# Performance work log

Measured on AMD Instinct MI355X. Metric: run time of the kernel, lower is better.

The kernel has to match this reference:

```python
import jax, jax.numpy as jnp
import numpy as np

TOPK = 8
N_EXPERTS = 64
ALPHA = 0.001


def setup_inputs() -> dict:
    key = jax.random.key(0)
    k1, k2 = jax.random.split(key)
    B, S, H = 4, 4096, 4096
    x = jax.random.normal(k1, (B, S, H), dtype=jnp.float32)
    # kaiming-uniform-ish router weight, bound = sqrt(6/((1+5)*H)) = 1/sqrt(H)
    bound = 1.0 / np.sqrt(H)
    weight = jax.random.uniform(k2, (N_EXPERTS, H), dtype=jnp.float32,
                                minval=-bound, maxval=bound)
    return {"x": x, "weight": weight}


def reference(x, weight):
    B, S, H = x.shape
    E = weight.shape[0]
    tokens = x.reshape(-1, H)                      # (T, H), T = B*S
    logits = jnp.einsum('th,eh->te', tokens, weight)  # router GEMM (T, E)
    scores = jax.nn.softmax(logits, axis=-1)
    # top-k selection (torch uses sorted=False; same set of values/indices)
    topk_weight, topk_idx = jax.lax.top_k(scores, TOPK)  # (T, k)
    # normalize top-k probs (norm_topk_prob=True, topk>1)
    topk_weight = topk_weight / (topk_weight.sum(axis=1, keepdims=True) + 1e-20)
    # seq-aux load-balancing loss (training path, alpha > 0, seq_aux=True)
    idx_flat = topk_idx.reshape(B, S * TOPK)                 # (B, S*k)
    ce = jax.nn.one_hot(idx_flat, E, dtype=jnp.float32).sum(axis=1)  # scatter_add of ones
    ce = ce / (S * TOPK / E)                                  # (B, E)
    mean_scores = scores.reshape(B, S, E).mean(axis=1)        # (B, E)
    aux_loss = (ce * mean_scores).sum(axis=1).mean() * ALPHA
    return topk_idx, topk_weight, aux_loss
```

## Files before the change

### kernel.cpp

```cpp
#include <hip/hip_runtime.h>
#include <math.h>

#define H 4096
#define NE 64
#define KTOP 8
#define BT 64
#define TTOT 16384
#define NBLK (TTOT / BT)
#define TAU 1e-4f
#define DELTA 1e-3f

typedef __attribute__((ext_vector_type(8))) short bf16x8;
typedef __attribute__((ext_vector_type(4))) float f32x4;

union U4S8 { uint4 u; bf16x8 s; };

__device__ __forceinline__ unsigned bf16_rne(float f) {
  unsigned b = __float_as_uint(f);
  b += 0x7fffu + ((b >> 16) & 1u);
  return b >> 16;
}

__global__ __launch_bounds__(256) void w_prep(const float* __restrict__ w,
                                              uint4* __restrict__ wsimg) {
  const int sid = blockIdx.x * 256 + threadIdx.x;
  const int e = sid >> 9;
  const int rem = sid & 511;
  const int c = rem >> 2;
  const int s = rem & 3;
  const float* src = w + (size_t)e * H + c * 32 + s * 8;
  float4 f0 = *(const float4*)src;
  float4 f1 = *(const float4*)(src + 4);
  float xf[8] = {f0.x, f0.y, f0.z, f0.w, f1.x, f1.y, f1.z, f1.w};
  unsigned hu[8], lu[8];
#pragma unroll
  for (int j = 0; j < 8; ++j) {
    hu[j] = bf16_rne(xf[j]);
    float hf = __uint_as_float(hu[j] << 16);
    lu[j] = bf16_rne(xf[j] - hf);
  }
  uint4 hp, lp;
  hp.x = hu[0] | (hu[1] << 16); hp.y = hu[2] | (hu[3] << 16);
  hp.z = hu[4] | (hu[5] << 16); hp.w = hu[6] | (hu[7] << 16);
  lp.x = lu[0] | (lu[1] << 16); lp.y = lu[2] | (lu[3] << 16);
  lp.z = lu[4] | (lu[5] << 16); lp.w = lu[6] | (lu[7] << 16);
  const int slotp = s ^ ((e >> 1) & 3);
  wsimg[(size_t)c * 256 + e * 4 + slotp] = hp;
  wsimg[(size_t)128 * 256 + (size_t)c * 256 + e * 4 + slotp] = lp;
}

struct __align__(16) SmemP1 {
  uint4 wbuf[2][1024];
  float lg[64 * 66];
  float msum[8][64];
  float cnt[8][64];
};

__global__ __launch_bounds__(512) void moe_pass1(
    const float* __restrict__ x, const uint4* __restrict__ wsimg,
    float* __restrict__ out, unsigned* __restrict__ wmask,
    float* __restrict__ waux) {
  __shared__ SmemP1 sm;
  const int tid = threadIdx.x;
  const int lane = tid & 63;
  const int wid = tid >> 6;
  const int tile = wid & 3;
  const int kh = wid >> 2;
  const int tok0 = blockIdx.x * BT;
  const int trow = lane & 15;
  const int kgrp = lane >> 4;

  const int sh = tid >> 8;
  const int shl = (tid >> 7) & 1;
  const int sfl = tid & 127;
  const uint4* simg = wsimg + (size_t)shl * (128 * 256);
  const int sdst = (sh * 2 + shl) * 256 + sfl * 2;

  const float* xp = x + (size_t)(tok0 + tile * 16 + trow) * H + kh * 2048 + kgrp * 8;

  int bidx[2][4];
#pragma unroll
  for (int hl = 0; hl < 2; ++hl)
#pragma unroll
    for (int et = 0; et < 4; ++et) {
      int e = et * 16 + trow;
      bidx[hl][et] = (kh * 2 + hl) * 256 + e * 4 + (kgrp ^ ((e >> 1) & 3));
    }

  f32x4 acc[4];
#pragma unroll
  for (int et = 0; et < 4; ++et) acc[et] = (f32x4){0.f, 0.f, 0.f, 0.f};

  {
    const int cg = sh ? 64 : 0;
    uint4 a = simg[(size_t)cg * 256 + sfl * 2];
    uint4 b = simg[(size_t)cg * 256 + sfl * 2 + 1];
    sm.wbuf[0][sdst] = a;
    sm.wbuf[0][sdst + 1] = b;
  }
  float4 xc0 = *(const float4*)(xp);
  float4 xc1 = *(const float4*)(xp + 4);
  __syncthreads();

#pragma unroll 1
  for (int c = 0; c < 64; ++c) {
    uint4 wg0, wg1;
    float4 xn0, xn1;
    const bool more = (c + 1) < 64;
    if (more) {
      const int cg = (sh ? 64 : 0) + c + 1;
      wg0 = simg[(size_t)cg * 256 + sfl * 2];
      wg1 = simg[(size_t)cg * 256 + sfl * 2 + 1];
      xn0 = *(const float4*)(xp + (c + 1) * 32);
      xn1 = *(const float4*)(xp + (c + 1) * 32 + 4);
    }
    const int buf = c & 1;
    U4S8 bh[4], bl[4];
#pragma unroll
    for (int et = 0; et < 4; ++et) {
      bh[et].u = sm.wbuf[buf][bidx[0][et]];
      bl[et].u = sm.wbuf[buf][bidx[1][et]];
    }
    float xf[8] = {xc0.x, xc0.y, xc0.z, xc0.w, xc1.x, xc1.y, xc1.z, xc1.w};
    unsigned ph[4], pl[4];
#pragma unroll
    for (int q = 0; q < 4; ++q)
      asm("v_cvt_pk_bf16_f32 %0, %1, %2" : "=v"(ph[q]) : "v"(xf[2 * q]), "v"(xf[2 * q + 1]));
    float rs[8];
#pragma unroll
    for (int q = 0; q < 4; ++q) {
      rs[2 * q]     = xf[2 * q]     - __uint_as_float(ph[q] << 16);
      rs[2 * q + 1] = xf[2 * q + 1] - __uint_as_float(ph[q] & 0xffff0000u);
    }
#pragma unroll
    for (int q = 0; q < 4; ++q)
      asm("v_cvt_pk_bf16_f32 %0, %1, %2" : "=v"(pl[q]) : "v"(rs[2 * q]), "v"(rs[2 * q + 1]));
    U4S8 ah, al;
    ah.u = (uint4){ph[0], ph[1], ph[2], ph[3]};
    al.u = (uint4){pl[0], pl[1], pl[2], pl[3]};
#pragma unroll
    for (int et = 0; et < 4; ++et) {
      acc[et] = __builtin_amdgcn_mfma_f32_16x16x32_bf16(ah.s, bh[et].s, acc[et], 0, 0, 0);
      acc[et] = __builtin_amdgcn_mfma_f32_16x16x32_bf16(ah.s, bl[et].s, acc[et], 0, 0, 0);
      acc[et] = __builtin_amdgcn_mfma_f32_16x16x32_bf16(al.s, bh[et].s, acc[et], 0, 0, 0);
    }
    if (more) {
      sm.wbuf[buf ^ 1][sdst] = wg0;
      sm.wbuf[buf ^ 1][sdst + 1] = wg1;
      xc0 = xn0; xc1 = xn1;
    }
    __syncthreads();
  }

  if (kh == 1) {
#pragma unroll
    for (int et = 0; et < 4; ++et)
#pragma unroll
      for (int r = 0; r < 4; ++r)
        sm.lg[(tile * 16 + kgrp * 4 + r) * 66 + et * 16 + trow] = acc[et][r];
  }
  __syncthreads();
  if (kh == 0) {
#pragma unroll
    for (int et = 0; et < 4; ++et)
#pragma unroll
      for (int r = 0; r < 4; ++r) {
        const int li = (tile * 16 + kgrp * 4 + r) * 66 + et * 16 + trow;
        sm.lg[li] += acc[et][r];
      }
  }
  __syncthreads();

  float msum = 0.f;
  int cnt = 0;
#pragma unroll 1
  for (int it = 0; it < 8; ++it) {
    const int t = wid * 8 + it;
    const float lf = sm.lg[t * 66 + lane];

    float m = lf;
#pragma unroll
    for (int off = 32; off; off >>= 1) m = fmaxf(m, __shfl_xor(m, off));
    float p = expf(lf - m);
    float s = p;
#pragma unroll
    for (int off = 32; off; off >>= 1) s += __shfl_xor(s, off);
    msum += p / s;

    float cur = lf;
    float myv = 0.f;
    int myi = 0;
#pragma unroll
    for (int r = 0; r < 9; ++r) {
      float v = cur;
      int ix = lane;
#pragma unroll
      for (int off = 1; off < 64; off <<= 1) {
        float ov = __shfl_xor(v, off);
        int oi = __shfl_xor(ix, off);
        if (ov > v || (ov == v && oi < ix)) { v = ov; ix = oi; }
      }
      if (lane == r) { myv = v; myi = ix; }
      if (r < 8 && lane == ix) { cur = -INFINITY; ++cnt; }
    }

    const float m0 = __shfl(myv, 0);
    float e = expf(myv - m0);
    float sv = e;
    sv += __shfl_xor(sv, 1);
    sv += __shfl_xor(sv, 2);
    sv += __shfl_xor(sv, 4);
    const float wgtv = e / sv;
    const int tg = tok0 + t;
    if (lane < KTOP) {
      out[(size_t)tg * KTOP + lane] = (float)myi;
      out[(size_t)TTOT * KTOP + (size_t)tg * KTOP + lane] = wgtv;
    }

    const float nxt = __shfl(myv, (lane + 1) & 63);
    const bool gp = (lane < 8) && (myv - nxt < TAU);
    const unsigned long long anyg = __ballot(gp);
    const float v7 = __shfl(myv, 7);
    const unsigned long long msk = __ballot(lf >= v7 - DELTA);
    if (lane == 0) {
      const unsigned long long mv = anyg ? msk : 0ULL;
      wmask[tg] = (unsigned)mv;
      wmask[TTOT + tg] = (unsigned)(mv >> 32);
    }
  }
  sm.msum[wid][lane] = msum;
  sm.cnt[wid][lane] = (float)cnt;
  __syncthreads();
  if (tid < 64) {
    float c8 = 0.f, m8 = 0.f;
#pragma unroll
    for (int k = 0; k < 8; ++k) { c8 += sm.cnt[k][tid]; m8 += sm.msum[k][tid]; }
    waux[blockIdx.x * 128 + tid] = c8;
    waux[blockIdx.x * 128 + 64 + tid] = m8;
  }
}

__global__ __launch_bounds__(256) void moe_pass2(
    const float* __restrict__ x, const float* __restrict__ w,
    const unsigned* __restrict__ wmask, float* __restrict__ out) {
  __shared__ unsigned slo[64], shi[64];
  __shared__ double red[4];
  __shared__ double cval[64];
  __shared__ int cidx[64];
  const int tid = threadIdx.x;
  const int lane = tid & 63, wid = tid >> 6;
  const int t0 = blockIdx.x * BT;

  if (tid < 64) { slo[tid] = wmask[t0 + tid]; shi[tid] = wmask[TTOT + t0 + tid]; }
  __syncthreads();
  int myf = (tid < 64) ? ((slo[tid] | shi[tid]) != 0u) : 0;
  if (!__syncthreads_or(myf)) return;

#pragma unroll 1
  for (int tt = 0; tt < BT; ++tt) {
    const unsigned lo = slo[tt], hi = shi[tt];
    if (!(lo | hi)) continue;
    const int t = t0 + tt;
    const unsigned long long m = ((unsigned long long)hi << 32) | lo;
    const float* xr = x + (size_t)t * H;
    int ncand = 0;
#pragma unroll 1
    for (int e = 0; e < 64; ++e) {
      if (!((m >> e) & 1ULL)) continue;
      const float* wr = w + (size_t)e * H;
      double d = 0.0;
#pragma unroll
      for (int q = 0; q < 16; ++q) {
        const int k = tid + 256 * q;
        d = fma((double)xr[k], (double)wr[k], d);
      }
#pragma unroll
      for (int off = 32; off; off >>= 1) d += __shfl_xor(d, off);
      if (lane == 0) red[wid] = d;
      __syncthreads();
      if (tid == 0) {
        cval[ncand] = red[0] + red[1] + red[2] + red[3];
        cidx[ncand] = e;
      }
      __syncthreads();
      ++ncand;
    }
    if (tid == 0) {
      double sel[8];
      int si[8];
      for (int r = 0; r < 8; ++r) {
        int best = 0;
        double bv = -1e300;
        for (int c2 = 0; c2 < ncand; ++c2)
          if (cval[c2] > bv) { bv = cval[c2]; best = c2; }
        sel[r] = cval[best]; si[r] = cidx[best];
        cval[best] = -1e301;
      }
      const double m0 = sel[0];
      float es[8], ssum = 0.f;
      for (int r = 0; r < 8; ++r) { es[r] = expf((float)(sel[r] - m0)); ssum += es[r]; }
      for (int r = 0; r < 8; ++r) {
        out[(size_t)t * KTOP + r] = (float)si[r];
        out[(size_t)TTOT * KTOP + (size_t)t * KTOP + r] = es[r] / ssum;
      }
    }
    __syncthreads();
  }
}

__global__ __launch_bounds__(256) void moe_gate_aux(
    const float* __restrict__ waux, float* __restrict__ out) {
  const int tid = threadIdx.x;
  const int b = tid >> 6, e = tid & 63;
  float cnt = 0.f, ms = 0.f;
#pragma unroll 4
  for (int j = 0; j < 64; ++j) {
    const int blk = b * 64 + j;
    cnt += waux[blk * 128 + e];
    ms += waux[blk * 128 + 64 + e];
  }
  float term = (cnt * (1.f / 512.f)) * (ms * (1.f / 4096.f));
  __shared__ float red[4];
#pragma unroll
  for (int off = 32; off; off >>= 1) term += __shfl_xor(term, off);
  if ((tid & 63) == 0) red[tid >> 6] = term;
  __syncthreads();
  if (tid == 0) {
    float tot = red[0] + red[1] + red[2] + red[3];
    out[(size_t)TTOT * KTOP * 2] = tot * (0.001f / 4.f);
  }
}

extern "C" void kernel_launch(void* const* d_in, const int* in_sizes, int n_in,
                              void* d_out, int out_size, void* d_ws, size_t ws_size,
                              hipStream_t stream) {
  (void)in_sizes; (void)n_in; (void)out_size; (void)ws_size;
  const float* x = (const float*)d_in[0];
  const float* w = (const float*)d_in[1];
  float* out = (float*)d_out;
  uint4* wsimg = (uint4*)d_ws;
  unsigned* wmask = (unsigned*)((char*)d_ws + (1 << 20));
  float* waux = (float*)((char*)d_ws + (1 << 20) + 2 * TTOT * 4);
  w_prep<<<128, 256, 0, stream>>>(w, wsimg);
  moe_pass1<<<NBLK, 512, 0, stream>>>(x, wsimg, out, wmask, waux);
  moe_pass2<<<NBLK, 256, 0, stream>>>(x, w, wmask, out);
  moe_gate_aux<<<1, 256, 0, stream>>>(waux, out);
}
```

Baseline: 204.8 us.

## Deepen pass1 prefetch pipeline with larger K-chunks and register-staged loads

The router GEMM main loop now processes two K-slices per barrier (32 iterations instead of 64). Weight tiles are prefetched two stages ahead in registers and x rows four stages ahead, and the shared weight buffer is doubled and unioned with the epilogue scratch. The barrier is issued through a raw s_waitcnt lgkmcnt plus s_barrier so it does not wait on outstanding global loads. This is meant to halve barrier count and hide global memory latency better, at the cost of more registers and LDS, which could reduce occupancy.

```diff
diff --git a/kernel.cpp b/kernel.cpp
--- a/kernel.cpp
+++ b/kernel.cpp
@@ -49,11 +49,34 @@
   wsimg[(size_t)128 * 256 + (size_t)c * 256 + e * 4 + slotp] = lp;
 }
 
-struct __align__(16) SmemP1 {
-  uint4 wbuf[2][1024];
-  float lg[64 * 66];
-  float msum[8][64];
-  float cnt[8][64];
+__device__ __forceinline__ void cvt_split(const float4 a, const float4 b,
+                                          bf16x8* hi, bf16x8* lo) {
+  float xf[8] = {a.x, a.y, a.z, a.w, b.x, b.y, b.z, b.w};
+  unsigned ph[4], pl[4];
+#pragma unroll
+  for (int q = 0; q < 4; ++q)
+    asm("v_cvt_pk_bf16_f32 %0, %1, %2" : "=v"(ph[q])
+        : "v"(xf[2 * q]), "v"(xf[2 * q + 1]));
+  float rs[8];
+#pragma unroll
+  for (int q = 0; q < 4; ++q) {
+    rs[2 * q]     = xf[2 * q]     - __uint_as_float(ph[q] << 16);
+    rs[2 * q + 1] = xf[2 * q + 1] - __uint_as_float(ph[q] & 0xffff0000u);
+  }
+#pragma unroll
+  for (int q = 0; q < 4; ++q)
+    asm("v_cvt_pk_bf16_f32 %0, %1, %2" : "=v"(pl[q])
+        : "v"(rs[2 * q]), "v"(rs[2 * q + 1]));
+  U4S8 h, l;
+  h.u = (uint4){ph[0], ph[1], ph[2], ph[3]};
+  l.u = (uint4){pl[0], pl[1], pl[2], pl[3]};
+  *hi = h.s;
+  *lo = l.s;
+}
+
+union __align__(16) SmemP1 {
+  uint4 wbuf[2][2048];
+  struct { float lg[64 * 66]; float msum[8][64]; float cnt[8][64]; } ep;
 };
 
 __global__ __launch_bounds__(512) void moe_pass1(
@@ -73,83 +96,95 @@
   const int sh = tid >> 8;
   const int shl = (tid >> 7) & 1;
   const int sfl = tid & 127;
-  const uint4* simg = wsimg + (size_t)shl * (128 * 256);
-  const int sdst = (sh * 2 + shl) * 256 + sfl * 2;
+  const uint4* simgp = wsimg + (size_t)shl * (128 * 256);
+  const int sbase = (sh * 2 + shl) * 256 + sfl * 2;
+  const int gbase = sh * 64;
 
   const float* xp = x + (size_t)(tok0 + tile * 16 + trow) * H + kh * 2048 + kgrp * 8;
 
-  int bidx[2][4];
-#pragma unroll
-  for (int hl = 0; hl < 2; ++hl)
-#pragma unroll
-    for (int et = 0; et < 4; ++et) {
-      int e = et * 16 + trow;
-      bidx[hl][et] = (kh * 2 + hl) * 256 + e * 4 + (kgrp ^ ((e >> 1) & 3));
-    }
+  int eoff[4];
+#pragma unroll
+  for (int et = 0; et < 4; ++et) {
+    const int e = et * 16 + trow;
+    eoff[et] = e * 4 + (kgrp ^ ((e >> 1) & 3));
+  }
+  const int kb = kh * 512;
 
   f32x4 acc[4];
 #pragma unroll
   for (int et = 0; et < 4; ++et) acc[et] = (f32x4){0.f, 0.f, 0.f, 0.f};
 
-  {
-    const int cg = sh ? 64 : 0;
-    uint4 a = simg[(size_t)cg * 256 + sfl * 2];
-    uint4 b = simg[(size_t)cg * 256 + sfl * 2 + 1];
-    sm.wbuf[0][sdst] = a;
-    sm.wbuf[0][sdst + 1] = b;
-  }
-  float4 xc0 = *(const float4*)(xp);
-  float4 xc1 = *(const float4*)(xp + 4);
+  uint4 wr[2][4];
+#pragma unroll
+  for (int p = 0; p < 2; ++p) {
+    const int g0 = gbase + p * 2;
+    wr[p][0] = simgp[(size_t)g0 * 256 + sfl * 2];
+    wr[p][1] = simgp[(size_t)g0 * 256 + sfl * 2 + 1];
+    wr[p][2] = simgp[(size_t)(g0 + 1) * 256 + sfl * 2];
+    wr[p][3] = simgp[(size_t)(g0 + 1) * 256 + sfl * 2 + 1];
+  }
+  float4 xb0[4][2], xb1[4][2];
+#pragma unroll
+  for (int d = 0; d < 4; ++d)
+#pragma unroll
+    for (int s = 0; s < 2; ++s) {
+      xb0[d][s] = *(const float4*)(xp + d * 64 + s * 32);
+      xb1[d][s] = *(const float4*)(xp + d * 64 + s * 32 + 4);
+    }
+  sm.wbuf[0][sbase]            = wr[0][0];
+  sm.wbuf[0][sbase + 1]        = wr[0][1];
+  sm.wbuf[0][1024 + sbase]     = wr[0][2];
+  sm.wbuf[0][1024 + sbase + 1] = wr[0][3];
   __syncthreads();
 
 #pragma unroll 1
-  for (int c = 0; c < 64; ++c) {
-    uint4 wg0, wg1;
-    float4 xn0, xn1;
-    const bool more = (c + 1) < 64;
-    if (more) {
-      const int cg = (sh ? 64 : 0) + c + 1;
-      wg0 = simg[(size_t)cg * 256 + sfl * 2];
-      wg1 = simg[(size_t)cg * 256 + sfl * 2 + 1];
-      xn0 = *(const float4*)(xp + (c + 1) * 32);
-      xn1 = *(const float4*)(xp + (c + 1) * 32 + 4);
-    }
-    const int buf = c & 1;
-    U4S8 bh[4], bl[4];
-#pragma unroll
-    for (int et = 0; et < 4; ++et) {
-      bh[et].u = sm.wbuf[buf][bidx[0][et]];
-      bl[et].u = sm.wbuf[buf][bidx[1][et]];
-    }
-    float xf[8] = {xc0.x, xc0.y, xc0.z, xc0.w, xc1.x, xc1.y, xc1.z, xc1.w};
-    unsigned ph[4], pl[4];
-#pragma unroll
-    for (int q = 0; q < 4; ++q)
-      asm("v_cvt_pk_bf16_f32 %0, %1, %2" : "=v"(ph[q]) : "v"(xf[2 * q]), "v"(xf[2 * q + 1]));
-    float rs[8];
-#pragma unroll
-    for (int q = 0; q < 4; ++q) {
-      rs[2 * q]     = xf[2 * q]     - __uint_as_float(ph[q] << 16);
-      rs[2 * q + 1] = xf[2 * q + 1] - __uint_as_float(ph[q] & 0xffff0000u);
-    }
-#pragma unroll
-    for (int q = 0; q < 4; ++q)
-      asm("v_cvt_pk_bf16_f32 %0, %1, %2" : "=v"(pl[q]) : "v"(rs[2 * q]), "v"(rs[2 * q + 1]));
-    U4S8 ah, al;
-    ah.u = (uint4){ph[0], ph[1], ph[2], ph[3]};
-    al.u = (uint4){pl[0], pl[1], pl[2], pl[3]};
-#pragma unroll
-    for (int et = 0; et < 4; ++et) {
-      acc[et] = __builtin_amdgcn_mfma_f32_16x16x32_bf16(ah.s, bh[et].s, acc[et], 0, 0, 0);
-      acc[et] = __builtin_amdgcn_mfma_f32_16x16x32_bf16(ah.s, bl[et].s, acc[et], 0, 0, 0);
-      acc[et] = __builtin_amdgcn_mfma_f32_16x16x32_bf16(al.s, bh[et].s, acc[et], 0, 0, 0);
-    }
-    if (more) {
-      sm.wbuf[buf ^ 1][sdst] = wg0;
-      sm.wbuf[buf ^ 1][sdst + 1] = wg1;
-      xc0 = xn0; xc1 = xn1;
-    }
-    __syncthreads();
+  for (int cb = 0; cb < 32; cb += 4) {
+#pragma unroll
+    for (int u = 0; u < 4; ++u) {
+      const int c = cb + u;
+      bf16x8 ah[2], al[2];
+      cvt_split(xb0[u][0], xb1[u][0], &ah[0], &al[0]);
+      cvt_split(xb0[u][1], xb1[u][1], &ah[1], &al[1]);
+      if (c + 2 < 32) {
+        const int g0 = gbase + (c + 2) * 2;
+        wr[u & 1][0] = simgp[(size_t)g0 * 256 + sfl * 2];
+        wr[u & 1][1] = simgp[(size_t)g0 * 256 + sfl * 2 + 1];
+        wr[u & 1][2] = simgp[(size_t)(g0 + 1) * 256 + sfl * 2];
+        wr[u & 1][3] = simgp[(size_t)(g0 + 1) * 256 + sfl * 2 + 1];
+      }
+      if (c + 4 < 32) {
+#pragma unroll
+        for (int s = 0; s < 2; ++s) {
+          xb0[u][s] = *(const float4*)(xp + (c + 4) * 64 + s * 32);
+          xb1[u][s] = *(const float4*)(xp + (c + 4) * 64 + s * 32 + 4);
+        }
+      }
+#pragma unroll
+      for (int s = 0; s < 2; ++s) {
+        U4S8 bh[4], bl[4];
+#pragma unroll
+        for (int et = 0; et < 4; ++et) {
+          bh[et].u = sm.wbuf[u & 1][s * 1024 + kb + eoff[et]];
+          bl[et].u = sm.wbuf[u & 1][s * 1024 + kb + 256 + eoff[et]];
+        }
+#pragma unroll
+        for (int et = 0; et < 4; ++et) {
+          acc[et] = __builtin_amdgcn_mfma_f32_16x16x32_bf16(ah[s], bh[et].s, acc[et], 0, 0, 0);
+          acc[et] = __builtin_amdgcn_mfma_f32_16x16x32_bf16(ah[s], bl[et].s, acc[et], 0, 0, 0);
+          acc[et] = __builtin_amdgcn_mfma_f32_16x16x32_bf16(al[s], bh[et].s, acc[et], 0, 0, 0);
+        }
+      }
+      if (c + 1 < 32) {
+        const int wd = (u + 1) & 1;
+        sm.wbuf[wd][sbase]            = wr[wd][0];
+        sm.wbuf[wd][sbase + 1]        = wr[wd][1];
+        sm.wbuf[wd][1024 + sbase]     = wr[wd][2];
+        sm.wbuf[wd][1024 + sbase + 1] = wr[wd][3];
+      }
+      asm volatile("s_waitcnt lgkmcnt(0)" ::: "memory");
+      __builtin_amdgcn_s_barrier();
+      asm volatile("" ::: "memory");
+    }
   }
 
   if (kh == 1) {
@@ -157,7 +192,7 @@
     for (int et = 0; et < 4; ++et)
 #pragma unroll
       for (int r = 0; r < 4; ++r)
-        sm.lg[(tile * 16 + kgrp * 4 + r) * 66 + et * 16 + trow] = acc[et][r];
+        sm.ep.lg[(tile * 16 + kgrp * 4 + r) * 66 + et * 16 + trow] = acc[et][r];
   }
   __syncthreads();
   if (kh == 0) {
@@ -166,7 +201,7 @@
 #pragma unroll
       for (int r = 0; r < 4; ++r) {
         const int li = (tile * 16 + kgrp * 4 + r) * 66 + et * 16 + trow;
-        sm.lg[li] += acc[et][r];
+        sm.ep.lg[li] += acc[et][r];
       }
   }
   __syncthreads();
@@ -176,7 +211,7 @@
 #pragma unroll 1
   for (int it = 0; it < 8; ++it) {
     const int t = wid * 8 + it;
-    const float lf = sm.lg[t * 66 + lane];
+    const float lf = sm.ep.lg[t * 66 + lane];
 
     float m = lf;
 #pragma unroll
@@ -228,13 +263,13 @@
       wmask[TTOT + tg] = (unsigned)(mv >> 32);
     }
   }
-  sm.msum[wid][lane] = msum;
-  sm.cnt[wid][lane] = (float)cnt;
+  sm.ep.msum[wid][lane] = msum;
+  sm.ep.cnt[wid][lane] = (float)cnt;
   __syncthreads();
   if (tid < 64) {
     float c8 = 0.f, m8 = 0.f;
 #pragma unroll
-    for (int k = 0; k < 8; ++k) { c8 += sm.cnt[k][tid]; m8 += sm.msum[k][tid]; }
+    for (int k = 0; k < 8; ++k) { c8 += sm.ep.cnt[k][tid]; m8 += sm.ep.msum[k][tid]; }
     waux[blockIdx.x * 128 + tid] = c8;
     waux[blockIdx.x * 128 + 64 + tid] = m8;
   }
```

Result: slower. 260.4 us (+27.2%).

## Stage x and weights via async global-to-LDS loads in 4-deep ring buffer

Applied to the files above, without the earlier changes.

Rewrites the router GEMM main loop to stream both the x tile and the bf16 hi/lo weight image directly into LDS with global_load_lds, using a 4-slot ring buffer and 3 steps of prefetch gated by vmcnt waits. The block shrinks from 512 to 256 threads, each wave owning 16 tokens across the full K range, which removes the split-K reduction through shared memory. x is read from LDS with an XOR swizzle and converted to bf16 hi/lo in registers. It uses 128 KB of dynamic LDS with one block per CU, which lowers occupancy and depends on the async pipeline to hide latency.

```diff
diff --git a/kernel.cpp b/kernel.cpp
--- a/kernel.cpp
+++ b/kernel.cpp
@@ -49,134 +49,139 @@
   wsimg[(size_t)128 * 256 + (size_t)c * 256 + e * 4 + slotp] = lp;
 }
 
-struct __align__(16) SmemP1 {
-  uint4 wbuf[2][1024];
-  float lg[64 * 66];
-  float msum[8][64];
-  float cnt[8][64];
-};
-
-__global__ __launch_bounds__(512) void moe_pass1(
+__device__ __forceinline__ void cvt_split(const float4 a, const float4 b,
+                                          bf16x8* hi, bf16x8* lo) {
+  float xf[8] = {a.x, a.y, a.z, a.w, b.x, b.y, b.z, b.w};
+  unsigned ph[4], pl[4];
+#pragma unroll
+  for (int q = 0; q < 4; ++q)
+    asm("v_cvt_pk_bf16_f32 %0, %1, %2" : "=v"(ph[q])
+        : "v"(xf[2 * q]), "v"(xf[2 * q + 1]));
+  float rs[8];
+#pragma unroll
+  for (int q = 0; q < 4; ++q) {
+    rs[2 * q]     = xf[2 * q]     - __uint_as_float(ph[q] << 16);
+    rs[2 * q + 1] = xf[2 * q + 1] - __uint_as_float(ph[q] & 0xffff0000u);
+  }
+#pragma unroll
+  for (int q = 0; q < 4; ++q)
+    asm("v_cvt_pk_bf16_f32 %0, %1, %2" : "=v"(pl[q])
+        : "v"(rs[2 * q]), "v"(rs[2 * q + 1]));
+  U4S8 h, l;
+  h.u = (uint4){ph[0], ph[1], ph[2], ph[3]};
+  l.u = (uint4){pl[0], pl[1], pl[2], pl[3]};
+  *hi = h.s;
+  *lo = l.s;
+}
+
+#define GLDS(GP, LP)                                                   \
+  __builtin_amdgcn_global_load_lds(                                    \
+      (const __attribute__((address_space(1))) void*)(GP),             \
+      (__attribute__((address_space(3))) void*)(LP), 16, 0, 0)
+
+__global__ __launch_bounds__(256, 1) void moe_pass1(
     const float* __restrict__ x, const uint4* __restrict__ wsimg,
     float* __restrict__ out, unsigned* __restrict__ wmask,
     float* __restrict__ waux) {
-  __shared__ SmemP1 sm;
+  extern __shared__ __align__(16) char smraw[];
   const int tid = threadIdx.x;
   const int lane = tid & 63;
   const int wid = tid >> 6;
-  const int tile = wid & 3;
-  const int kh = wid >> 2;
   const int tok0 = blockIdx.x * BT;
   const int trow = lane & 15;
   const int kgrp = lane >> 4;
 
-  const int sh = tid >> 8;
-  const int shl = (tid >> 7) & 1;
-  const int sfl = tid & 127;
-  const uint4* simg = wsimg + (size_t)shl * (128 * 256);
-  const int sdst = (sh * 2 + shl) * 256 + sfl * 2;
-
-  const float* xp = x + (size_t)(tok0 + tile * 16 + trow) * H + kh * 2048 + kgrp * 8;
-
-  int bidx[2][4];
-#pragma unroll
-  for (int hl = 0; hl < 2; ++hl)
-#pragma unroll
-    for (int et = 0; et < 4; ++et) {
-      int e = et * 16 + trow;
-      bidx[hl][et] = (kh * 2 + hl) * 256 + e * 4 + (kgrp ^ ((e >> 1) & 3));
-    }
+  const char* xsrc[4];
+#pragma unroll
+  for (int j = 0; j < 4; ++j) {
+    const int Lb = j * 4096 + tid * 16;
+    const int row = Lb >> 8;
+    const int inrow = Lb & 255;
+    const int sin = inrow ^ ((row & 7) << 4);
+    xsrc[j] = (const char*)(x + (size_t)(tok0 + row) * H) + sin;
+  }
+  const uint4* wsrc[4];
+#pragma unroll
+  for (int j = 0; j < 4; ++j)
+    wsrc[j] = wsimg + (size_t)(j >> 1) * (128 * 256) + (j & 1) * 256 + tid;
 
   f32x4 acc[4];
 #pragma unroll
   for (int et = 0; et < 4; ++et) acc[et] = (f32x4){0.f, 0.f, 0.f, 0.f};
 
-  {
-    const int cg = sh ? 64 : 0;
-    uint4 a = simg[(size_t)cg * 256 + sfl * 2];
-    uint4 b = simg[(size_t)cg * 256 + sfl * 2 + 1];
-    sm.wbuf[0][sdst] = a;
-    sm.wbuf[0][sdst + 1] = b;
-  }
-  float4 xc0 = *(const float4*)(xp);
-  float4 xc1 = *(const float4*)(xp + 4);
-  __syncthreads();
+#define ISSUE_STEP(KC, BUF)                                             \
+  do {                                                                  \
+    char* bb = smraw + (BUF) * 32768 + (wid << 10);                     \
+    _Pragma("unroll") for (int j = 0; j < 4; ++j)                       \
+      GLDS(xsrc[j] + (size_t)(KC) * 256, bb + j * 4096);                \
+    _Pragma("unroll") for (int j = 0; j < 4; ++j)                       \
+      GLDS((const char*)(wsrc[j] + (size_t)(KC) * 512),                 \
+           bb + 16384 + j * 4096);                                      \
+  } while (0)
+
+  ISSUE_STEP(0, 0);
+  ISSUE_STEP(1, 1);
+  ISSUE_STEP(2, 2);
+
+  const int arow = wid * 16 + trow;
+  const int sx = (trow & 7) << 4;
+  const int abase = arow * 256 + kgrp * 32;
+  int entry[4];
+#pragma unroll
+  for (int et = 0; et < 4; ++et) {
+    const int e = et * 16 + trow;
+    entry[et] = (e * 4 + (kgrp ^ ((e >> 1) & 3))) * 16;
+  }
 
 #pragma unroll 1
-  for (int c = 0; c < 64; ++c) {
-    uint4 wg0, wg1;
-    float4 xn0, xn1;
-    const bool more = (c + 1) < 64;
-    if (more) {
-      const int cg = (sh ? 64 : 0) + c + 1;
-      wg0 = simg[(size_t)cg * 256 + sfl * 2];
-      wg1 = simg[(size_t)cg * 256 + sfl * 2 + 1];
-      xn0 = *(const float4*)(xp + (c + 1) * 32);
-      xn1 = *(const float4*)(xp + (c + 1) * 32 + 4);
-    }
-    const int buf = c & 1;
-    U4S8 bh[4], bl[4];
-#pragma unroll
-    for (int et = 0; et < 4; ++et) {
-      bh[et].u = sm.wbuf[buf][bidx[0][et]];
-      bl[et].u = sm.wbuf[buf][bidx[1][et]];
-    }
-    float xf[8] = {xc0.x, xc0.y, xc0.z, xc0.w, xc1.x, xc1.y, xc1.z, xc1.w};
-    unsigned ph[4], pl[4];
-#pragma unroll
-    for (int q = 0; q < 4; ++q)
-      asm("v_cvt_pk_bf16_f32 %0, %1, %2" : "=v"(ph[q]) : "v"(xf[2 * q]), "v"(xf[2 * q + 1]));
-    float rs[8];
-#pragma unroll
-    for (int q = 0; q < 4; ++q) {
-      rs[2 * q]     = xf[2 * q]     - __uint_as_float(ph[q] << 16);
-      rs[2 * q + 1] = xf[2 * q + 1] - __uint_as_float(ph[q] & 0xffff0000u);
-    }
-#pragma unroll
-    for (int q = 0; q < 4; ++q)
-      asm("v_cvt_pk_bf16_f32 %0, %1, %2" : "=v"(pl[q]) : "v"(rs[2 * q]), "v"(rs[2 * q + 1]));
-    U4S8 ah, al;
-    ah.u = (uint4){ph[0], ph[1], ph[2], ph[3]};
-    al.u = (uint4){pl[0], pl[1], pl[2], pl[3]};
-#pragma unroll
-    for (int et = 0; et < 4; ++et) {
-      acc[et] = __builtin_amdgcn_mfma_f32_16x16x32_bf16(ah.s, bh[et].s, acc[et], 0, 0, 0);
-      acc[et] = __builtin_amdgcn_mfma_f32_16x16x32_bf16(ah.s, bl[et].s, acc[et], 0, 0, 0);
-      acc[et] = __builtin_amdgcn_mfma_f32_16x16x32_bf16(al.s, bh[et].s, acc[et], 0, 0, 0);
-    }
-    if (more) {
-      sm.wbuf[buf ^ 1][sdst] = wg0;
-      sm.wbuf[buf ^ 1][sdst + 1] = wg1;
-      xc0 = xn0; xc1 = xn1;
-    }
-    __syncthreads();
-  }
-
-  if (kh == 1) {
-#pragma unroll
-    for (int et = 0; et < 4; ++et)
-#pragma unroll
-      for (int r = 0; r < 4; ++r)
-        sm.lg[(tile * 16 + kgrp * 4 + r) * 66 + et * 16 + trow] = acc[et][r];
-  }
-  __syncthreads();
-  if (kh == 0) {
-#pragma unroll
-    for (int et = 0; et < 4; ++et)
-#pragma unroll
-      for (int r = 0; r < 4; ++r) {
-        const int li = (tile * 16 + kgrp * 4 + r) * 66 + et * 16 + trow;
-        sm.lg[li] += acc[et][r];
-      }
-  }
+  for (int kc = 0; kc < 64; ++kc) {
+    if (kc < 62) {
+      asm volatile("s_waitcnt vmcnt(16)" ::: "memory");
+    } else if (kc == 62) {
+      asm volatile("s_waitcnt vmcnt(8)" ::: "memory");
+    } else {
+      asm volatile("s_waitcnt vmcnt(0)" ::: "memory");
+    }
+    __builtin_amdgcn_s_barrier();
+    asm volatile("" ::: "memory");
+    if (kc + 3 < 64) ISSUE_STEP(kc + 3, (kc + 3) & 3);
+
+    const char* bufp = smraw + (kc & 3) * 32768;
+#pragma unroll
+    for (int sub = 0; sub < 2; ++sub) {
+      float4 v0 = *(const float4*)(bufp + ((abase + sub * 128) ^ sx));
+      float4 v1 = *(const float4*)(bufp + ((abase + sub * 128 + 16) ^ sx));
+      bf16x8 ah, al;
+      cvt_split(v0, v1, &ah, &al);
+#pragma unroll
+      for (int et = 0; et < 4; ++et) {
+        U4S8 bh, bl;
+        bh.u = *(const uint4*)(bufp + 16384 + sub * 4096 + entry[et]);
+        bl.u = *(const uint4*)(bufp + 16384 + (2 + sub) * 4096 + entry[et]);
+        acc[et] = __builtin_amdgcn_mfma_f32_16x16x32_bf16(ah, bh.s, acc[et], 0, 0, 0);
+        acc[et] = __builtin_amdgcn_mfma_f32_16x16x32_bf16(ah, bl.s, acc[et], 0, 0, 0);
+        acc[et] = __builtin_amdgcn_mfma_f32_16x16x32_bf16(al, bh.s, acc[et], 0, 0, 0);
+      }
+    }
+  }
+
+  __syncthreads();
+  float* lg = (float*)smraw;
+  float* msumA = (float*)(smraw + 16896);
+  float* cntA = (float*)(smraw + 17920);
+#pragma unroll
+  for (int et = 0; et < 4; ++et)
+#pragma unroll
+    for (int r = 0; r < 4; ++r)
+      lg[(wid * 16 + kgrp * 4 + r) * 66 + et * 16 + trow] = acc[et][r];
   __syncthreads();
 
   float msum = 0.f;
   int cnt = 0;
 #pragma unroll 1
-  for (int it = 0; it < 8; ++it) {
-    const int t = wid * 8 + it;
-    const float lf = sm.lg[t * 66 + lane];
+  for (int it = 0; it < 16; ++it) {
+    const int t = wid * 16 + it;
+    const float lf = lg[t * 66 + lane];
 
     float m = lf;
 #pragma unroll
@@ -228,15 +233,18 @@
       wmask[TTOT + tg] = (unsigned)(mv >> 32);
     }
   }
-  sm.msum[wid][lane] = msum;
-  sm.cnt[wid][lane] = (float)cnt;
+  msumA[wid * 64 + lane] = msum;
+  cntA[wid * 64 + lane] = (float)cnt;
   __syncthreads();
   if (tid < 64) {
-    float c8 = 0.f, m8 = 0.f;
-#pragma unroll
-    for (int k = 0; k < 8; ++k) { c8 += sm.cnt[k][tid]; m8 += sm.msum[k][tid]; }
-    waux[blockIdx.x * 128 + tid] = c8;
-    waux[blockIdx.x * 128 + 64 + tid] = m8;
+    float c4 = 0.f, m4 = 0.f;
+#pragma unroll
+    for (int k = 0; k < 4; ++k) {
+      c4 += cntA[k * 64 + tid];
+      m4 += msumA[k * 64 + tid];
+    }
+    waux[blockIdx.x * 128 + tid] = c4;
+    waux[blockIdx.x * 128 + 64 + tid] = m4;
   }
 }
 
@@ -339,10 +347,12 @@
   const float* w = (const float*)d_in[1];
   float* out = (float*)d_out;
   uint4* wsimg = (uint4*)d_ws;
-  unsigned* wmask = (unsigned*)((char*)d_ws + (1 << 20));
-  float* waux = (float*)((char*)d_ws + (1 << 20) + 2 * TTOT * 4);
+  unsigned* wmask = (unsigned*)((char*)d_ws + (1 << 21));
+  float* waux = (float*)((char*)d_ws + (1 << 21) + 2 * TTOT * 4);
+  (void)hipFuncSetAttribute((const void*)moe_pass1,
+                            hipFuncAttributeMaxDynamicSharedMemorySize, 131072);
   w_prep<<<128, 256, 0, stream>>>(w, wsimg);
-  moe_pass1<<<NBLK, 512, 0, stream>>>(x, wsimg, out, wmask, waux);
+  moe_pass1<<<NBLK, 256, 131072, stream>>>(x, wsimg, out, wmask, waux);
   moe_pass2<<<NBLK, 256, 0, stream>>>(x, w, wmask, out);
   moe_gate_aux<<<1, 256, 0, stream>>>(waux, out);
 }
```

After: 240.2 us. 1.17x slower.
